# Kernel optimization log

Hardware: AMD Instinct MI355X
Metric: run time of the kernel (lower is better)

The kernel has to match this reference:

```python
import jax, jax.numpy as jnp
import numpy as np

N = 30000      # nodes
E = 480000     # edges
F = 128        # num_node_features (== C, required by LSTM-JK stacking of h_list incl. x)
C = 128        # graph_hidden_channels
K = 8          # kernel_size (num gaussians)
D = 2          # pseudo-coordinate dim
L = 4          # nlayers
H = (L * C) // 2   # PyG JK-LSTM hidden size = 256
NHID = 512
NOUT = 256
B = 1024       # number of graphs in batch
EPS = 1e-15


def setup_inputs() -> dict:
    key = jax.random.key(0)
    ks = jax.random.split(key, 24)
    s = 0.05
    inp = {}
    inp['x'] = jax.random.normal(ks[0], (N, F), jnp.float32)
    inp['edge_index'] = jax.random.randint(ks[1], (2, E), 0, N, dtype=jnp.int32)
    inp['edge_attr'] = jax.random.uniform(ks[2], (E, D), jnp.float32)
    inp['batch'] = jnp.sort(jax.random.randint(ks[3], (N,), 0, B, dtype=jnp.int32))
    # GMMConv params per layer (Cin == C for all layers since F == C)
    inp['g'] = jax.random.normal(ks[4], (L, F, K * C), jnp.float32) * s
    inp['root'] = jax.random.normal(ks[5], (L, F, C), jnp.float32) * s
    inp['bias'] = jnp.zeros((L, C), jnp.float32)
    inp['mu'] = jax.random.uniform(ks[6], (L, K, D), jnp.float32)
    inp['sigma'] = jax.random.uniform(ks[7], (L, K, D), jnp.float32) * 0.5 + 0.5
    inp['bn_gamma'] = jnp.ones((L, C), jnp.float32)
    inp['bn_beta'] = jnp.zeros((L, C), jnp.float32)
    # Bidirectional LSTM for JumpingKnowledge: dir 0 = fwd, dir 1 = bwd; gate order i,f,g,o
    inp['w_ih'] = jax.random.normal(ks[8], (2, 4 * H, C), jnp.float32) * s
    inp['w_hh'] = jax.random.normal(ks[9], (2, 4 * H, H), jnp.float32) * s
    inp['b_ih'] = jnp.zeros((2, 4 * H), jnp.float32)
    inp['b_hh'] = jnp.zeros((2, 4 * H), jnp.float32)
    inp['att_w'] = jax.random.normal(ks[10], (2 * H, 1), jnp.float32) * s
    inp['att_b'] = jnp.zeros((1,), jnp.float32)
    inp['p1_w'] = jax.random.normal(ks[11], (C, NHID), jnp.float32) * s
    inp['p1_b'] = jnp.zeros((NHID,), jnp.float32)
    inp['p2_w'] = jax.random.normal(ks[12], (NHID, NOUT), jnp.float32) * s
    inp['p2_b'] = jnp.zeros((NOUT,), jnp.float32)
    inp['ln_g'] = jnp.ones((NOUT,), jnp.float32)
    inp['ln_b'] = jnp.zeros((NOUT,), jnp.float32)
    return inp


def _lstm_dir(xs, w_ih, w_hh, b_ih, b_hh, reverse):
    # xs: [T, N, C] -> hidden states [T, N, H], aligned with input order
    def step(carry, xt):
        h, c = carry
        gates = xt @ w_ih.T + h @ w_hh.T + (b_ih + b_hh)
        i, f, g, o = jnp.split(gates, 4, axis=-1)
        c = jax.nn.sigmoid(f) * c + jax.nn.sigmoid(i) * jnp.tanh(g)
        h = jax.nn.sigmoid(o) * jnp.tanh(c)
        return (h, c), h
    h0 = jnp.zeros((xs.shape[1], w_hh.shape[1]), xs.dtype)
    _, hs = jax.lax.scan(step, (h0, h0), xs, reverse=reverse)
    return hs


def reference(x, edge_index, edge_attr, batch, g, root, bias, mu, sigma,
              bn_gamma, bn_beta, w_ih, w_hh, b_ih, b_hh, att_w, att_b,
              p1_w, p1_b, p2_w, p2_b, ln_g, ln_b):
    src, dst = edge_index[0], edge_index[1]
    deg = jnp.maximum(jax.ops.segment_sum(jnp.ones((E,), x.dtype), dst, num_segments=N), 1.0)[:, None]
    h = x
    h_list = [x]
    for i in range(L):
        # GMMConv: node-level transform then gaussian-weighted message passing (mean aggr)
        xg = (h @ g[i]).reshape(N, K, C)                     # [N, K, C]
        diff = edge_attr[:, None, :] - mu[i][None]           # [E, K, D]
        w = jnp.exp(jnp.sum(-0.5 * diff ** 2 / (EPS + sigma[i][None] ** 2), axis=-1))  # [E, K]
        msg = jnp.zeros((E, C), x.dtype)
        for k in range(K):                                   # small fixed K; avoids [E,K,C] gather
            msg = msg + w[:, k:k + 1] * xg[src, k, :]
        agg = jax.ops.segment_sum(msg, dst, num_segments=N) / deg
        h = agg + h @ root[i] + bias[i]
        # BatchNorm1d (training-mode batch statistics)
        mean = h.mean(0)
        var = h.var(0)
        h = (h - mean) / jnp.sqrt(var + 1e-5) * bn_gamma[i] + bn_beta[i]
        if i < L - 1:
            h = jax.nn.relu(h)
        # dropout is identity in eval mode
        h_list.append(h)
    # JumpingKnowledge, mode='lstm'
    xs = jnp.stack(h_list, axis=0)                           # [L+1, N, C]
    hf = _lstm_dir(xs, w_ih[0], w_hh[0], b_ih[0], b_hh[0], False)
    hb = _lstm_dir(xs, w_ih[1], w_hh[1], b_ih[1], b_hh[1], True)
    seq = jnp.concatenate([hf, hb], axis=-1)                 # [L+1, N, 2H]
    alpha = (seq @ att_w)[..., 0] + att_b[0]                 # [L+1, N]
    alpha = jax.nn.softmax(alpha, axis=0)
    node_rep = jnp.sum(alpha[..., None] * xs, axis=0)        # [N, C]
    # global_mean_pool
    cnt = jnp.maximum(jax.ops.segment_sum(jnp.ones((N,), x.dtype), batch, num_segments=B), 1.0)
    h_graph = jax.ops.segment_sum(node_rep, batch, num_segments=B) / cnt[:, None]
    z = jax.nn.relu(h_graph @ p1_w + p1_b)
    z = z @ p2_w + p2_b
    zm = z.mean(-1, keepdims=True)
    zv = z.var(-1, keepdims=True)
    return (z - zm) / jnp.sqrt(zv + 1e-5) * ln_g + ln_b
```

## Files before the change

kernel.cpp:

```cpp
#include <hip/hip_runtime.h>
#include <hip/hip_bf16.h>
#include <math.h>

#define N_    30000
#define E_    480000
#define C_    128
#define K_    8
#define L_    4
#define H_    256
#define NHID_ 512
#define NOUT_ 256
#define B_    1024
#define SCAN_B 30

typedef __attribute__((ext_vector_type(8))) short short8;
typedef __attribute__((ext_vector_type(4))) float floatx4;
typedef __hip_bfloat16 bf16;

static inline size_t align256(size_t x){ return (x + 255) & ~(size_t)255; }

__device__ __forceinline__ void gload_lds16(const void* g, void* l){
  __builtin_amdgcn_global_load_lds((const __attribute__((address_space(1))) void*)g,
                                   (__attribute__((address_space(3))) void*)l, 16, 0, 0);
}
__device__ __forceinline__ float bf2f(short s){
  union { unsigned u; float f; } x; x.u = ((unsigned)(unsigned short)s) << 16; return x.f;
}
__device__ __forceinline__ float sigm_f(float x){ return __builtin_amdgcn_rcpf(1.f + __expf(-x)); }
__device__ __forceinline__ float tanh_f(float x){ return 1.f - 2.f*__builtin_amdgcn_rcpf(1.f + __expf(2.f*x)); }

__global__ void hist_k(const int* __restrict__ dst, int* __restrict__ cnt){
  int e = blockIdx.x*256 + threadIdx.x;
  if (e < E_) atomicAdd(&cnt[dst[e]], 1);
}

__global__ void scan1_k(const int* __restrict__ cnt, int* __restrict__ rowptr, int* __restrict__ btot){
  __shared__ int sh[1024];
  int i = blockIdx.x*1024 + (int)threadIdx.x;
  int v = (i < N_) ? cnt[i] : 0;
  sh[threadIdx.x] = v;
  __syncthreads();
  for (int o = 1; o < 1024; o <<= 1){
    int t = (threadIdx.x >= (unsigned)o) ? sh[threadIdx.x - o] : 0;
    __syncthreads();
    sh[threadIdx.x] += t;
    __syncthreads();
  }
  if (i < N_) rowptr[i] = sh[threadIdx.x] - v;
  if (threadIdx.x == 1023) btot[blockIdx.x] = sh[1023];
}
__global__ void scan2_k(const int* __restrict__ btot, int* __restrict__ boff){
  if (threadIdx.x == 0){
    int s = 0;
    for (int b = 0; b < SCAN_B; b++){ boff[b] = s; s += btot[b]; }
    boff[SCAN_B] = s;
  }
}
__global__ void scan3_k(int* __restrict__ rowptr, const int* __restrict__ boff){
  int i = blockIdx.x*1024 + (int)threadIdx.x;
  if (i < N_) rowptr[i] += boff[blockIdx.x];
  if (i == N_-1) rowptr[N_] = boff[SCAN_B];
}

__global__ void degf_k(const int* __restrict__ cnt, float* __restrict__ degf){
  int n = blockIdx.x*256 + threadIdx.x;
  if (n < N_) degf[n] = fmaxf((float)cnt[n], 1.0f);
}

__global__ void scatter_k(const int* __restrict__ src, const int* __restrict__ dst,
                          const float* __restrict__ ea,
                          const int* __restrict__ rowptr, int* __restrict__ fill,
                          int* __restrict__ srcsort, float* __restrict__ easort){
  int e = blockIdx.x*256 + threadIdx.x;
  if (e >= E_) return;
  int d = dst[e];
  int pos = rowptr[d] + atomicAdd(&fill[d], 1);
  srcsort[pos] = src[e];
  ((float2*)easort)[pos] = ((const float2*)ea)[e];
}

__global__ void cast_k(const float* __restrict__ in, bf16* __restrict__ out, int n){
  int i = blockIdx.x*256 + threadIdx.x;
  if (i < n) out[i] = __float2bfloat16(in[i]);
}
__global__ void tcast_k(const float* __restrict__ in, bf16* __restrict__ out, int R, int Cc){
  const float* ip = in + (size_t)blockIdx.y*R*Cc;
  bf16* op = out + (size_t)blockIdx.y*R*Cc;
  int i = blockIdx.x*256 + threadIdx.x;
  if (i >= R*Cc) return;
  int c = i / R, r = i - c*R;
  op[i] = __float2bfloat16(ip[(size_t)r*Cc + c]);
}
__global__ void gtcast_k(const float* __restrict__ in, bf16* __restrict__ out){
  const float* ip = in + (size_t)blockIdx.y*C_*(K_*C_);
  bf16* op = out + (size_t)blockIdx.y*C_*(K_*C_);
  int i = blockIdx.x*256 + threadIdx.x;
  int co = i >> 10;
  int rem = i & 1023;
  int k = rem >> 7, c = rem & 127;
  op[i] = __float2bfloat16(ip[(size_t)c*(K_*C_) + k*C_ + co]);
}
__global__ void permcast_k(const float* __restrict__ in, bf16* __restrict__ out, int Kdim){
  const float* ip = in + (size_t)blockIdx.y*1024*Kdim;
  bf16* op = out + (size_t)blockIdx.y*1024*Kdim;
  int i = blockIdx.x*256 + threadIdx.x;
  if (i >= 1024*Kdim) return;
  int r = i / Kdim, k = i - r*Kdim;
  int gsel = r >> 8, jj = r & 255;
  int p = ((jj >> 5) << 7) + (((jj >> 4) & 1) << 6) + (gsel << 4) + (jj & 15);
  op[(size_t)p*Kdim + k] = __float2bfloat16(ip[i]);
}
__global__ void biassum_k(const float* __restrict__ bih, const float* __restrict__ bhh,
                          float* __restrict__ bs){
  int i = blockIdx.x*256 + threadIdx.x;
  if (i < 2048) bs[i] = bih[i] + bhh[i];
}

template<int OUTBF16>
__global__ __launch_bounds__(256)
void gemm_bf16_k(const bf16* __restrict__ A1, const bf16* __restrict__ B1, int K1,
                 const bf16* __restrict__ A2, const bf16* __restrict__ B2, int K2,
                 const float* __restrict__ bias1,
                 void* __restrict__ Cout, int M, int Nn, int relu)
{
  __shared__ short As[128*32];
  __shared__ short Bs[128*32];
  const int tid  = threadIdx.x;
  const int wave = tid >> 6, lane = tid & 63;
  const int m0 = blockIdx.y*128, n0 = blockIdx.x*128;
  const int wm = (wave >> 1)*64, wn = (wave & 1)*64;
  const int lrow = lane & 15, lk = lane >> 4;
  floatx4 acc[4][4] = {};

  #pragma unroll
  for (int phase = 0; phase < 2; ++phase){
    const bf16* A = phase ? A2 : A1;
    const bf16* B = phase ? B2 : B1;
    const int   K = phase ? K2 : K1;
    if (A == nullptr) continue;
    for (int k0 = 0; k0 < K; k0 += 32){
      #pragma unroll
      for (int i = 0; i < 2; ++i){
        const int c    = i*256 + wave*64 + lane;
        const int row  = c >> 2;
        const int jsrc = (c & 3) ^ ((c >> 3) & 3);
        int ar = m0 + row; if (ar >= M) ar = M - 1;
        gload_lds16(A + (size_t)ar*K + k0 + jsrc*8,         As + (size_t)c*8);
        gload_lds16(B + (size_t)(n0 + row)*K + k0 + jsrc*8, Bs + (size_t)c*8);
      }
      __syncthreads();
      short8 af[4], bfr[4];
      #pragma unroll
      for (int t = 0; t < 4; ++t){
        const int ra = wm + t*16 + lrow;
        const int rb = wn + t*16 + lrow;
        af[t]  = *(const short8*)&As[(ra*4 + (lk ^ ((ra >> 1) & 3)))*8];
        bfr[t] = *(const short8*)&Bs[(rb*4 + (lk ^ ((rb >> 1) & 3)))*8];
      }
      #pragma unroll
      for (int mt = 0; mt < 4; ++mt)
        #pragma unroll
        for (int nt = 0; nt < 4; ++nt)
          acc[mt][nt] = __builtin_amdgcn_mfma_f32_16x16x32_bf16(af[mt], bfr[nt], acc[mt][nt], 0, 0, 0);
      __syncthreads();
    }
  }

  float* outf = (float*)Cout;
  bf16*  outb = (bf16*)Cout;
  #pragma unroll
  for (int nt = 0; nt < 4; ++nt){
    const int col = n0 + wn + nt*16 + lrow;
    float bv = bias1 ? bias1[col] : 0.f;
    #pragma unroll
    for (int mt = 0; mt < 4; ++mt){
      #pragma unroll
      for (int r = 0; r < 4; ++r){
        const int row = m0 + wm + mt*16 + lk*4 + r;
        if (row >= M) continue;
        float v = acc[mt][nt][r] + bv;
        if (relu) v = fmaxf(v, 0.f);
        if (OUTBF16) outb[(size_t)row*Nn + col] = __float2bfloat16(v);
        else         outf[(size_t)row*Nn + col] = v;
      }
    }
  }
}

__global__ __launch_bounds__(256)
void gmm_gemm64_k(const bf16* __restrict__ tbuf, const bf16* __restrict__ gGTl,
                  const bf16* __restrict__ hin, const bf16* __restrict__ rootTl,
                  const float* __restrict__ bias, float* __restrict__ outp,
                  float* __restrict__ stats, int M)
{
  __shared__ short As[128*64];
  __shared__ short Bs[128*64];
  __shared__ float colstat[256];
  const int tid  = threadIdx.x;
  const int wave = tid >> 6, lane = tid & 63;
  const int m0 = blockIdx.x*128;
  const int wm = (wave >> 1)*64, wn = (wave & 1)*64;
  const int lrow = lane & 15, lk = lane >> 4;
  floatx4 acc[4][4] = {};
  colstat[tid] = 0.f;

  #pragma unroll
  for (int phase = 0; phase < 2; ++phase){
    const bf16* A  = phase ? hin    : tbuf;
    const bf16* B  = phase ? rootTl : gGTl;
    const int   ld = phase ? C_     : (K_*C_);
    const int   K  = phase ? C_     : (K_*C_);
    for (int k0 = 0; k0 < K; k0 += 64){
      #pragma unroll
      for (int i = 0; i < 4; ++i){
        const int c    = i*256 + wave*64 + lane;
        const int row  = c >> 3;
        const int jsrc = (c & 7) ^ (row & 7);
        int ar = m0 + row; if (ar >= M) ar = M - 1;
        gload_lds16(A + (size_t)ar*ld + k0 + jsrc*8,  As + (size_t)c*8);
        gload_lds16(B + (size_t)row*ld + k0 + jsrc*8, Bs + (size_t)c*8);
      }
      __syncthreads();
      #pragma unroll
      for (int kk = 0; kk < 2; ++kk){
        short8 af[4], bfr[4];
        #pragma unroll
        for (int t = 0; t < 4; ++t){
          const int ra = wm + t*16 + lrow;
          const int rb = wn + t*16 + lrow;
          af[t]  = *(const short8*)&As[(ra*8 + ((kk*4 + lk) ^ (ra & 7)))*8];
          bfr[t] = *(const short8*)&Bs[(rb*8 + ((kk*4 + lk) ^ (rb & 7)))*8];
        }
        #pragma unroll
        for (int mt = 0; mt < 4; ++mt)
          #pragma unroll
          for (int nt = 0; nt < 4; ++nt)
            acc[mt][nt] = __builtin_amdgcn_mfma_f32_16x16x32_bf16(af[mt], bfr[nt], acc[mt][nt], 0, 0, 0);
      }
      __syncthreads();
    }
  }

  #pragma unroll
  for (int nt = 0; nt < 4; ++nt){
    const int col = wn + nt*16 + lrow;
    const float bv = bias[col];
    float s = 0.f, s2 = 0.f;
    #pragma unroll
    for (int mt = 0; mt < 4; ++mt){
      #pragma unroll
      for (int r = 0; r < 4; ++r){
        const int row = m0 + wm + mt*16 + lk*4 + r;
        if (row >= M) continue;
        float v = acc[mt][nt][r] + bv;
        outp[(size_t)row*C_ + col] = v;
        s += v; s2 += v*v;
      }
    }
    s  += __shfl_down(s, 16);  s  += __shfl_down(s, 32);
    s2 += __shfl_down(s2, 16); s2 += __shfl_down(s2, 32);
    if (lane < 16){
      atomicAdd(&colstat[wn + nt*16 + lane], s);
      atomicAdd(&colstat[128 + wn + nt*16 + lane], s2);
    }
  }
  __syncthreads();
  if (tid < 128){
    atomicAdd(&stats[tid],       colstat[tid]);
    atomicAdd(&stats[128 + tid], colstat[128 + tid]);
  }
}

__global__ __launch_bounds__(256)
void lstm_step2_k(const bf16* __restrict__ A1f, const bf16* __restrict__ A1b,
                  const bf16* __restrict__ wihp, const bf16* __restrict__ whhp,
                  const bf16* __restrict__ hpf, const bf16* __restrict__ hpb,
                  const float* __restrict__ bsum,
                  bf16* __restrict__ hof, bf16* __restrict__ hob,
                  bf16* __restrict__ csf, bf16* __restrict__ csb,
                  const float* __restrict__ attw,
                  float* __restrict__ alf, float* __restrict__ alb,
                  int M)
{
  __shared__ short As[128*32];
  __shared__ short Bs[128*32];
  const int dir = blockIdx.z;
  const bf16* A1 = dir ? A1b : A1f;
  const bf16* A2 = dir ? hpb : hpf;
  const bf16* B1 = wihp + (size_t)dir*4*H_*C_;
  const bf16* B2 = whhp + (size_t)dir*4*H_*H_;
  bf16* hout = dir ? hob : hof;
  bf16* cst  = dir ? csb : csf;
  float* alpha = dir ? alb : alf;
  const float* bsd = bsum + (size_t)dir*4*H_;
  const float* awd = attw + (size_t)dir*H_;

  const int tid  = threadIdx.x;
  const int wave = tid >> 6, lane = tid & 63;
  const int m0 = blockIdx.y*128, n0 = blockIdx.x*128;
  const int wm = (wave >> 1)*64, wn = (wave & 1)*64;
  const int lrow = lane & 15, lk = lane >> 4;
  floatx4 acc[4][4] = {};

  #pragma unroll
  for (int phase = 0; phase < 2; ++phase){
    const bf16* A = phase ? A2 : A1;
    const bf16* B = phase ? B2 : B1;
    const int   K = phase ? H_ : C_;
    if (A == nullptr) continue;
    for (int k0 = 0; k0 < K; k0 += 32){
      #pragma unroll
      for (int i = 0; i < 2; ++i){
        const int c    = i*256 + wave*64 + lane;
        const int row  = c >> 2;
        const int jsrc = (c & 3) ^ ((c >> 3) & 3);
        int ar = m0 + row; if (ar >= M) ar = M - 1;
        gload_lds16(A + (size_t)ar*K + k0 + jsrc*8,         As + (size_t)c*8);
        gload_lds16(B + (size_t)(n0 + row)*K + k0 + jsrc*8, Bs + (size_t)c*8);
      }
      __syncthreads();
      short8 af[4], bfr[4];
      #pragma unroll
      for (int t = 0; t < 4; ++t){
        const int ra = wm + t*16 + lrow;
        const int rb = wn + t*16 + lrow;
        af[t]  = *(const short8*)&As[(ra*4 + (lk ^ ((ra >> 1) & 3)))*8];
        bfr[t] = *(const short8*)&Bs[(rb*4 + (lk ^ ((rb >> 1) & 3)))*8];
      }
      #pragma unroll
      for (int mt = 0; mt < 4; ++mt)
        #pragma unroll
        for (int nt = 0; nt < 4; ++nt)
          acc[mt][nt] = __builtin_amdgcn_mfma_f32_16x16x32_bf16(af[mt], bfr[nt], acc[mt][nt], 0, 0, 0);
      __syncthreads();
    }
  }

  const int j  = blockIdx.x*32 + (wave & 1)*16 + lrow;
  const float bi = bsd[0*H_ + j], bff = bsd[1*H_ + j];
  const float bg = bsd[2*H_ + j], bo  = bsd[3*H_ + j];
  const float aw = awd[j];
  #pragma unroll
  for (int mt = 0; mt < 4; ++mt){
    #pragma unroll
    for (int r = 0; r < 4; ++r){
      const int row = m0 + wm + mt*16 + lk*4 + r;
      const bool ok = row < M;
      const size_t idx = (size_t)row*H_ + j;
      float co = 0.f;
      if (A2 && ok) co = __bfloat162float(cst[idx]);
      float ig = sigm_f(acc[mt][0][r] + bi);
      float fg = sigm_f(acc[mt][1][r] + bff);
      float gt = tanh_f(acc[mt][2][r] + bg);
      float og = sigm_f(acc[mt][3][r] + bo);
      float cv = fg*co + ig*gt;
      float hv = og*tanh_f(cv);
      if (ok && hout){
        cst[idx]  = __float2bfloat16(cv);
        hout[idx] = __float2bfloat16(hv);
      }
      float att = ok ? hv*aw : 0.f;
      att += __shfl_xor(att, 1);
      att += __shfl_xor(att, 2);
      att += __shfl_xor(att, 4);
      att += __shfl_xor(att, 8);
      if (lrow == 0 && ok) atomicAdd(&alpha[row], att);
    }
  }
}

__global__ void compute_w_k(const float* __restrict__ easort, const float* __restrict__ mu,
                            const float* __restrict__ sigma, bf16* __restrict__ wsrt)
{
  int e = blockIdx.x*256 + threadIdx.x;
  if (e >= E_) return;
  float2 a = ((const float2*)easort)[e];
  short8 o;
  #pragma unroll
  for (int k = 0; k < 8; k++){
    float d0 = a.x - mu[2*k],  d1 = a.y - mu[2*k+1];
    float s0 = sigma[2*k],     s1 = sigma[2*k+1];
    float t = -0.5f*(d0*d0/(1e-15f + s0*s0) + d1*d1/(1e-15f + s1*s1));
    o[k] = __builtin_bit_cast(short, __float2bfloat16(expf(t)));
  }
  *(short8*)(wsrt + (size_t)e*8) = o;
}

__global__ __launch_bounds__(256)
void aggregate_t_k(const bf16* __restrict__ h, const bf16* __restrict__ wsrt,
                   const int* __restrict__ rowptr, const int* __restrict__ srcsort,
                   const float* __restrict__ degf, bf16* __restrict__ t)
{
  int node = blockIdx.x*4 + (threadIdx.x >> 6);
  int lane = threadIdx.x & 63;
  if (node >= N_) return;
  int p0 = rowptr[node], p1 = rowptr[node+1];
  float ax[8] = {}, ay[8] = {};
  for (int p = p0; p < p1; p++){
    int s = srcsort[p];
    short8 wv = *(const short8*)(wsrt + (size_t)p*8);
    float2 v = __bfloat1622float2(((const __hip_bfloat162*)(h + (size_t)s*C_))[lane]);
    #pragma unroll
    for (int k = 0; k < 8; k++){
      float wk = bf2f(wv[k]);
      ax[k] = fmaf(wk, v.x, ax[k]);
      ay[k] = fmaf(wk, v.y, ay[k]);
    }
  }
  float inv = 1.0f / degf[node];
  __hip_bfloat162* tp = (__hip_bfloat162*)(t + (size_t)node*(K_*C_));
  #pragma unroll
  for (int k = 0; k < 8; k++){
    __hip_bfloat162 o; o.x = __float2bfloat16(ax[k]*inv); o.y = __float2bfloat16(ay[k]*inv);
    tp[k*64 + lane] = o;
  }
}

__global__ void bn_apply_k(const float* __restrict__ hpre, const float* __restrict__ stats,
                           const float* __restrict__ gamma, const float* __restrict__ beta,
                           bf16* __restrict__ outp, int relu)
{
  int i = blockIdx.x*256 + threadIdx.x;
  if (i >= N_*C_) return;
  int c = i & 127;
  float mean = stats[c] * (1.0f/N_);
  float var  = stats[c+128] * (1.0f/N_) - mean*mean;
  float rstd = rsqrtf(var + 1e-5f);
  float v = (hpre[i] - mean)*rstd*gamma[c] + beta[c];
  if (relu) v = fmaxf(v, 0.f);
  outp[i] = __float2bfloat16(v);
}

__global__ void jk_pool_k(const float* __restrict__ x, const bf16* __restrict__ hlist,
                          const float* __restrict__ alpha, const int* __restrict__ batch,
                          float* __restrict__ hgraph, float* __restrict__ gcnt)
{
  int n = blockIdx.x, c = threadIdx.x;
  float a[5]; float mx = -1e30f;
  #pragma unroll
  for (int t = 0; t < 5; t++){ a[t] = alpha[(size_t)t*N_ + n]; mx = fmaxf(mx, a[t]); }
  float ssum = 0.f;
  #pragma unroll
  for (int t = 0; t < 5; t++){ a[t] = expf(a[t] - mx); ssum += a[t]; }
  float inv = 1.0f/ssum;
  float val = a[0]*inv*x[(size_t)n*C_ + c];
  #pragma unroll
  for (int t = 1; t < 5; t++)
    val = fmaf(a[t]*inv, __bfloat162float(hlist[((size_t)(t-1)*N_ + n)*C_ + c]), val);
  int bg = batch[n];
  atomicAdd(&hgraph[(size_t)bg*C_ + c], val);
  if (c == 0) atomicAdd(&gcnt[bg], 1.0f);
}

__global__ void pool_div_k(const float* __restrict__ hg, const float* __restrict__ gcnt,
                           bf16* __restrict__ hgb){
  int i = blockIdx.x*256 + threadIdx.x;
  if (i < B_*C_) hgb[i] = __float2bfloat16(hg[i] / fmaxf(gcnt[i >> 7], 1.0f));
}

__global__ __launch_bounds__(256)
void layernorm_k(float* __restrict__ z, const float* __restrict__ g, const float* __restrict__ b){
  int row = blockIdx.x, j = threadIdx.x;
  float v = z[(size_t)row*NOUT_ + j];
  float s = v, s2 = v*v;
  #pragma unroll
  for (int o = 32; o; o >>= 1){ s += __shfl_down(s, o); s2 += __shfl_down(s2, o); }
  __shared__ float sh[8];
  int w = j >> 6;
  if ((j & 63) == 0){ sh[w] = s; sh[4+w] = s2; }
  __syncthreads();
  float st  = sh[0] + sh[1] + sh[2] + sh[3];
  float st2 = sh[4] + sh[5] + sh[6] + sh[7];
  float mean = st * (1.0f/NOUT_);
  float var  = st2 * (1.0f/NOUT_) - mean*mean;
  float rstd = rsqrtf(var + 1e-5f);
  z[(size_t)row*NOUT_ + j] = (v - mean)*rstd*g[j] + b[j];
}

extern "C" void kernel_launch(void* const* d_in, const int* in_sizes, int n_in,
                              void* d_out, int out_size, void* d_ws, size_t ws_size,
                              hipStream_t stream)
{
  (void)in_sizes; (void)n_in; (void)out_size; (void)ws_size;
  const float* x     = (const float*)d_in[0];
  const int*   eidx  = (const int*)  d_in[1];
  const float* eattr = (const float*)d_in[2];
  const int*   batch = (const int*)  d_in[3];
  const float* g     = (const float*)d_in[4];
  const float* root  = (const float*)d_in[5];
  const float* bias  = (const float*)d_in[6];
  const float* mu    = (const float*)d_in[7];
  const float* sigma = (const float*)d_in[8];
  const float* bng   = (const float*)d_in[9];
  const float* bnb   = (const float*)d_in[10];
  const float* w_ih  = (const float*)d_in[11];
  const float* w_hh  = (const float*)d_in[12];
  const float* b_ih  = (const float*)d_in[13];
  const float* b_hh  = (const float*)d_in[14];
  const float* attw  = (const float*)d_in[15];
  const float* p1w   = (const float*)d_in[17];
  const float* p1b   = (const float*)d_in[18];
  const float* p2w   = (const float*)d_in[19];
  const float* p2b   = (const float*)d_in[20];
  const float* lng   = (const float*)d_in[21];
  const float* lnb   = (const float*)d_in[22];
  float* outp = (float*)d_out;

  const int* src = eidx;
  const int* dst = eidx + E_;

  size_t off = 0;
  char* wsb = (char*)d_ws;
  auto carve = [&](size_t bytes)->void*{ void* p = wsb + off; off = align256(off + bytes); return p; };
  bf16*  hlist  = (bf16*) carve((size_t)L_*N_*C_*2);
  void*  big    =         carve((size_t)N_*(K_*C_)*2);
  void*  uni    =         carve((size_t)6*N_*H_*2 + 256);
  bf16*  xb     = (bf16*) carve((size_t)N_*C_*2);
  float* alpha  = (float*)carve((size_t)(L_+1)*N_*4);
  float* hgraph = (float*)carve((size_t)B_*C_*4);
  bf16*  hgb    = (bf16*) carve((size_t)B_*C_*2);
  float* gcnt   = (float*)carve((size_t)B_*4);
  bf16*  z1b    = (bf16*) carve((size_t)B_*NHID_*2);
  float* bnstats= (float*)carve((size_t)L_*2*C_*4);
  float* degf   = (float*)carve((size_t)N_*4);
  int* cnt      = (int*)  carve((size_t)N_*4);
  int* rowptr   = (int*)  carve((size_t)(N_+1)*4);
  int* fill     = (int*)  carve((size_t)N_*4);
  int* srcsort  = (int*)  carve((size_t)E_*4);
  float* easort = (float*)carve((size_t)E_*2*4);
  int* btot     = (int*)  carve((size_t)(SCAN_B+1)*4);
  int* boff     = (int*)  carve((size_t)(SCAN_B+1)*4);
  bf16* gGT   = (bf16*)carve((size_t)L_*C_*(K_*C_)*2);
  bf16* rootT = (bf16*)carve((size_t)L_*C_*C_*2);
  bf16* wihp  = (bf16*)carve((size_t)2*4*H_*C_*2);
  bf16* whhp  = (bf16*)carve((size_t)2*4*H_*H_*2);
  float* bsum = (float*)carve((size_t)2*4*H_*4);
  bf16* p1T   = (bf16*)carve((size_t)NHID_*C_*2);
  bf16* p2T   = (bf16*)carve((size_t)NOUT_*NHID_*2);

  bf16*  wsrt   = (bf16*)uni;
  float* hpre   = (float*)((char*)uni + (size_t)E_*K_*2);
  bf16*  hAf    = (bf16*)uni;
  bf16*  hAb    = hAf + (size_t)N_*H_;
  bf16*  hBf    = hAb + (size_t)N_*H_;
  bf16*  hBb    = hBf + (size_t)N_*H_;
  bf16*  csf    = hBb + (size_t)N_*H_;
  bf16*  csb    = csf + (size_t)N_*H_;
  bf16*  tbuf   = (bf16*)big;

  hipMemsetAsync(cnt,     0, (size_t)N_*4, stream);
  hipMemsetAsync(fill,    0, (size_t)N_*4, stream);
  hipMemsetAsync(bnstats, 0, (size_t)L_*2*C_*4, stream);
  hipMemsetAsync(hgraph,  0, (size_t)B_*C_*4, stream);
  hipMemsetAsync(gcnt,    0, (size_t)B_*4, stream);
  hipMemsetAsync(alpha,   0, (size_t)(L_+1)*N_*4, stream);

  const dim3 blk(256);

  hist_k  <<<(E_+255)/256, 256, 0, stream>>>(dst, cnt);
  scan1_k <<<SCAN_B, 1024, 0, stream>>>(cnt, rowptr, btot);
  scan2_k <<<1, 64, 0, stream>>>(btot, boff);
  scan3_k <<<SCAN_B, 1024, 0, stream>>>(rowptr, boff);
  degf_k  <<<(N_+255)/256, 256, 0, stream>>>(cnt, degf);
  scatter_k<<<(E_+255)/256, 256, 0, stream>>>(src, dst, eattr, rowptr, fill, srcsort, easort);

  cast_k <<<(N_*C_+255)/256, blk, 0, stream>>>(x, xb, N_*C_);
  gtcast_k<<<dim3((C_*K_*C_)/256, L_), blk, 0, stream>>>(g, gGT);
  tcast_k<<<dim3((C_*C_+255)/256,   L_), blk, 0, stream>>>(root, rootT, C_,   C_);
  permcast_k<<<dim3((1024*C_+255)/256, 2), blk, 0, stream>>>(w_ih, wihp, C_);
  permcast_k<<<dim3((1024*H_+255)/256, 2), blk, 0, stream>>>(w_hh, whhp, H_);
  biassum_k<<<8, blk, 0, stream>>>(b_ih, b_hh, bsum);
  tcast_k<<<dim3((C_*NHID_+255)/256, 1), blk, 0, stream>>>(p1w, p1T, C_,    NHID_);
  tcast_k<<<dim3((NHID_*NOUT_+255)/256,1), blk, 0, stream>>>(p2w, p2T, NHID_, NOUT_);

  const int MB = (N_ + 127)/128;

  for (int l = 0; l < L_; l++){
    const bf16* hin = l ? (hlist + (size_t)(l-1)*N_*C_) : xb;
    compute_w_k<<<(E_+255)/256, blk, 0, stream>>>(easort, mu + (size_t)l*K_*2, sigma + (size_t)l*K_*2, wsrt);
    aggregate_t_k<<<N_/4, blk, 0, stream>>>(hin, wsrt, rowptr, srcsort, degf, tbuf);
    gmm_gemm64_k<<<dim3(MB), blk, 0, stream>>>(
        tbuf, gGT + (size_t)l*C_*K_*C_, hin, rootT + (size_t)l*C_*C_,
        bias + (size_t)l*C_, hpre, bnstats + l*2*C_, N_);
    bn_apply_k<<<(N_*C_+255)/256, blk, 0, stream>>>(hpre, bnstats + l*2*C_, bng + (size_t)l*C_, bnb + (size_t)l*C_,
                                                    hlist + (size_t)l*N_*C_, (l < L_-1) ? 1 : 0);
  }

  {
    const bf16 *hpf = nullptr, *hpb = nullptr;
    for (int s = 0; s < 5; s++){
      int tf = s, tb = 4 - s;
      const bf16* xtf = tf ? (hlist + (size_t)(tf-1)*N_*C_) : xb;
      const bf16* xtb = tb ? (hlist + (size_t)(tb-1)*N_*C_) : xb;
      bf16* hof = (s == 4) ? nullptr : ((s & 1) ? hBf : hAf);
      bf16* hob = (s == 4) ? nullptr : ((s & 1) ? hBb : hAb);
      lstm_step2_k<<<dim3(8, MB, 2), blk, 0, stream>>>(
          xtf, xtb, wihp, whhp, hpf, hpb, bsum, hof, hob, csf, csb,
          attw, alpha + (size_t)tf*N_, alpha + (size_t)tb*N_, N_);
      hpf = hof; hpb = hob;
    }
  }

  jk_pool_k<<<N_, 128, 0, stream>>>(x, hlist, alpha, batch, hgraph, gcnt);
  pool_div_k<<<(B_*C_+255)/256, blk, 0, stream>>>(hgraph, gcnt, hgb);

  gemm_bf16_k<1><<<dim3(NHID_/128, B_/128), blk, 0, stream>>>(
      hgb, p1T, C_, nullptr, nullptr, 0, p1b, z1b, B_, NHID_, 1);
  gemm_bf16_k<0><<<dim3(NOUT_/128, B_/128), blk, 0, stream>>>(
      z1b, p2T, NHID_, nullptr, nullptr, 0, p2b, outp, B_, NOUT_, 0);
  layernorm_k<<<B_, 256, 0, stream>>>(outp, lng, lnb);
}
```

Before: 1.213 ms.

## Halve GMM GEMM row tile, batch edge weights for all layers, fuse degf

The GMM GEMM tile shrinks from 128 to 64 rows per block, with each wave covering all 64 rows and 32 columns. That roughly doubles the grid (about 469 blocks instead of 235) and gives the 256 CUs more work to spread across, at the cost of more B-tile reloads per output. The Gaussian edge weights for all four layers are now computed in one kernel before the layer loop, saving three launches but using four times the scratch memory in the union buffer. The degf computation is folded into scan1_k, which removes one more launch.

```diff
diff --git a/kernel.cpp b/kernel.cpp
--- a/kernel.cpp
+++ b/kernel.cpp
@@ -34,10 +34,12 @@
   if (e < E_) atomicAdd(&cnt[dst[e]], 1);
 }
 
-__global__ void scan1_k(const int* __restrict__ cnt, int* __restrict__ rowptr, int* __restrict__ btot){
+__global__ void scan1_k(const int* __restrict__ cnt, int* __restrict__ rowptr,
+                        int* __restrict__ btot, float* __restrict__ degf){
   __shared__ int sh[1024];
   int i = blockIdx.x*1024 + (int)threadIdx.x;
   int v = (i < N_) ? cnt[i] : 0;
+  if (i < N_) degf[i] = fmaxf((float)v, 1.0f);
   sh[threadIdx.x] = v;
   __syncthreads();
   for (int o = 1; o < 1024; o <<= 1){
@@ -60,11 +62,6 @@
   int i = blockIdx.x*1024 + (int)threadIdx.x;
   if (i < N_) rowptr[i] += boff[blockIdx.x];
   if (i == N_-1) rowptr[N_] = boff[SCAN_B];
-}
-
-__global__ void degf_k(const int* __restrict__ cnt, float* __restrict__ degf){
-  int n = blockIdx.x*256 + threadIdx.x;
-  if (n < N_) degf[n] = fmaxf((float)cnt[n], 1.0f);
 }
 
 __global__ void scatter_k(const int* __restrict__ src, const int* __restrict__ dst,
@@ -193,15 +190,15 @@
                   const float* __restrict__ bias, float* __restrict__ outp,
                   float* __restrict__ stats, int M)
 {
-  __shared__ short As[128*64];
+  __shared__ short As[64*64];
   __shared__ short Bs[128*64];
   __shared__ float colstat[256];
   const int tid  = threadIdx.x;
   const int wave = tid >> 6, lane = tid & 63;
-  const int m0 = blockIdx.x*128;
-  const int wm = (wave >> 1)*64, wn = (wave & 1)*64;
+  const int m0 = blockIdx.x*64;
+  const int wn = wave*32;
   const int lrow = lane & 15, lk = lane >> 4;
-  floatx4 acc[4][4] = {};
+  floatx4 acc[4][2] = {};
   colstat[tid] = 0.f;
 
   #pragma unroll
@@ -212,47 +209,53 @@
     const int   K  = phase ? C_     : (K_*C_);
     for (int k0 = 0; k0 < K; k0 += 64){
       #pragma unroll
-      for (int i = 0; i < 4; ++i){
-        const int c    = i*256 + wave*64 + lane;
-        const int row  = c >> 3;
-        const int jsrc = (c & 7) ^ (row & 7);
-        int ar = m0 + row; if (ar >= M) ar = M - 1;
-        gload_lds16(A + (size_t)ar*ld + k0 + jsrc*8,  As + (size_t)c*8);
-        gload_lds16(B + (size_t)row*ld + k0 + jsrc*8, Bs + (size_t)c*8);
+      for (int i = 0; i < 6; ++i){
+        const int t = i*256 + wave*64 + lane;
+        if (t < 512){
+          const int c = t, row = c >> 3, jsrc = (c & 7) ^ (row & 7);
+          int ar = m0 + row; if (ar >= M) ar = M - 1;
+          gload_lds16(A + (size_t)ar*ld + k0 + jsrc*8, As + (size_t)c*8);
+        } else {
+          const int c = t - 512, row = c >> 3, jsrc = (c & 7) ^ (row & 7);
+          gload_lds16(B + (size_t)row*ld + k0 + jsrc*8, Bs + (size_t)c*8);
+        }
       }
       __syncthreads();
       #pragma unroll
       for (int kk = 0; kk < 2; ++kk){
-        short8 af[4], bfr[4];
+        short8 af[4], bfr[2];
         #pragma unroll
         for (int t = 0; t < 4; ++t){
-          const int ra = wm + t*16 + lrow;
-          const int rb = wn + t*16 + lrow;
-          af[t]  = *(const short8*)&As[(ra*8 + ((kk*4 + lk) ^ (ra & 7)))*8];
-          bfr[t] = *(const short8*)&Bs[(rb*8 + ((kk*4 + lk) ^ (rb & 7)))*8];
+          const int ra = t*16 + lrow;
+          af[t] = *(const short8*)&As[(ra*8 + ((kk*4 + lk) ^ (ra & 7)))*8];
+        }
+        #pragma unroll
+        for (int u = 0; u < 2; ++u){
+          const int rb = wn + u*16 + lrow;
+          bfr[u] = *(const short8*)&Bs[(rb*8 + ((kk*4 + lk) ^ (rb & 7)))*8];
         }
         #pragma unroll
         for (int mt = 0; mt < 4; ++mt)
           #pragma unroll
-          for (int nt = 0; nt < 4; ++nt)
-            acc[mt][nt] = __builtin_amdgcn_mfma_f32_16x16x32_bf16(af[mt], bfr[nt], acc[mt][nt], 0, 0, 0);
+          for (int u = 0; u < 2; ++u)
+            acc[mt][u] = __builtin_amdgcn_mfma_f32_16x16x32_bf16(af[mt], bfr[u], acc[mt][u], 0, 0, 0);
       }
       __syncthreads();
     }
   }
 
   #pragma unroll
-  for (int nt = 0; nt < 4; ++nt){
-    const int col = wn + nt*16 + lrow;
+  for (int u = 0; u < 2; ++u){
+    const int col = wn + u*16 + lrow;
     const float bv = bias[col];
     float s = 0.f, s2 = 0.f;
     #pragma unroll
     for (int mt = 0; mt < 4; ++mt){
       #pragma unroll
       for (int r = 0; r < 4; ++r){
-        const int row = m0 + wm + mt*16 + lk*4 + r;
+        const int row = m0 + mt*16 + lk*4 + r;
         if (row >= M) continue;
-        float v = acc[mt][nt][r] + bv;
+        float v = acc[mt][u][r] + bv;
         outp[(size_t)row*C_ + col] = v;
         s += v; s2 += v*v;
       }
@@ -260,8 +263,8 @@
     s  += __shfl_down(s, 16);  s  += __shfl_down(s, 32);
     s2 += __shfl_down(s2, 16); s2 += __shfl_down(s2, 32);
     if (lane < 16){
-      atomicAdd(&colstat[wn + nt*16 + lane], s);
-      atomicAdd(&colstat[128 + wn + nt*16 + lane], s2);
+      atomicAdd(&colstat[col], s);
+      atomicAdd(&colstat[128 + col], s2);
     }
   }
   __syncthreads();
@@ -369,21 +372,24 @@
   }
 }
 
-__global__ void compute_w_k(const float* __restrict__ easort, const float* __restrict__ mu,
-                            const float* __restrict__ sigma, bf16* __restrict__ wsrt)
+__global__ void compute_w4_k(const float* __restrict__ easort, const float* __restrict__ mu,
+                             const float* __restrict__ sigma, bf16* __restrict__ wsrt4)
 {
   int e = blockIdx.x*256 + threadIdx.x;
   if (e >= E_) return;
   float2 a = ((const float2*)easort)[e];
-  short8 o;
-  #pragma unroll
-  for (int k = 0; k < 8; k++){
-    float d0 = a.x - mu[2*k],  d1 = a.y - mu[2*k+1];
-    float s0 = sigma[2*k],     s1 = sigma[2*k+1];
-    float t = -0.5f*(d0*d0/(1e-15f + s0*s0) + d1*d1/(1e-15f + s1*s1));
-    o[k] = __builtin_bit_cast(short, __float2bfloat16(expf(t)));
-  }
-  *(short8*)(wsrt + (size_t)e*8) = o;
+  #pragma unroll
+  for (int l = 0; l < L_; l++){
+    short8 o;
+    #pragma unroll
+    for (int k = 0; k < 8; k++){
+      float d0 = a.x - mu[l*16 + 2*k],  d1 = a.y - mu[l*16 + 2*k+1];
+      float s0 = sigma[l*16 + 2*k],     s1 = sigma[l*16 + 2*k+1];
+      float t = -0.5f*(d0*d0/(1e-15f + s0*s0) + d1*d1/(1e-15f + s1*s1));
+      o[k] = __builtin_bit_cast(short, __float2bfloat16(expf(t)));
+    }
+    *(short8*)(wsrt4 + ((size_t)l*E_ + e)*8) = o;
+  }
 }
 
 __global__ __launch_bounds__(256)
@@ -538,8 +544,8 @@
   bf16* p1T   = (bf16*)carve((size_t)NHID_*C_*2);
   bf16* p2T   = (bf16*)carve((size_t)NOUT_*NHID_*2);
 
-  bf16*  wsrt   = (bf16*)uni;
-  float* hpre   = (float*)((char*)uni + (size_t)E_*K_*2);
+  bf16*  wsrt4  = (bf16*)uni;
+  float* hpre   = (float*)((char*)uni + (size_t)L_*E_*K_*2);
   bf16*  hAf    = (bf16*)uni;
   bf16*  hAb    = hAf + (size_t)N_*H_;
   bf16*  hBf    = hAb + (size_t)N_*H_;
@@ -558,10 +564,9 @@
   const dim3 blk(256);
 
   hist_k  <<<(E_+255)/256, 256, 0, stream>>>(dst, cnt);
-  scan1_k <<<SCAN_B, 1024, 0, stream>>>(cnt, rowptr, btot);
+  scan1_k <<<SCAN_B, 1024, 0, stream>>>(cnt, rowptr, btot, degf);
   scan2_k <<<1, 64, 0, stream>>>(btot, boff);
   scan3_k <<<SCAN_B, 1024, 0, stream>>>(rowptr, boff);
-  degf_k  <<<(N_+255)/256, 256, 0, stream>>>(cnt, degf);
   scatter_k<<<(E_+255)/256, 256, 0, stream>>>(src, dst, eattr, rowptr, fill, srcsort, easort);
 
   cast_k <<<(N_*C_+255)/256, blk, 0, stream>>>(x, xb, N_*C_);
@@ -573,13 +578,15 @@
   tcast_k<<<dim3((C_*NHID_+255)/256, 1), blk, 0, stream>>>(p1w, p1T, C_,    NHID_);
   tcast_k<<<dim3((NHID_*NOUT_+255)/256,1), blk, 0, stream>>>(p2w, p2T, NHID_, NOUT_);
 
+  compute_w4_k<<<(E_+255)/256, blk, 0, stream>>>(easort, mu, sigma, wsrt4);
+
   const int MB = (N_ + 127)/128;
+  const int MB64 = (N_ + 63)/64;
 
   for (int l = 0; l < L_; l++){
     const bf16* hin = l ? (hlist + (size_t)(l-1)*N_*C_) : xb;
-    compute_w_k<<<(E_+255)/256, blk, 0, stream>>>(easort, mu + (size_t)l*K_*2, sigma + (size_t)l*K_*2, wsrt);
-    aggregate_t_k<<<N_/4, blk, 0, stream>>>(hin, wsrt, rowptr, srcsort, degf, tbuf);
-    gmm_gemm64_k<<<dim3(MB), blk, 0, stream>>>(
+    aggregate_t_k<<<N_/4, blk, 0, stream>>>(hin, wsrt4 + (size_t)l*E_*K_, rowptr, srcsort, degf, tbuf);
+    gmm_gemm64_k<<<dim3(MB64), blk, 0, stream>>>(
         tbuf, gGT + (size_t)l*C_*K_*C_, hin, rootT + (size_t)l*C_*C_,
         bias + (size_t)l*C_, hpre, bnstats + l*2*C_, N_);
     bn_apply_k<<<(N_*C_+255)/256, blk, 0, stream>>>(hpre, bnstats + l*2*C_, bng + (size_t)l*C_, bnb + (size_t)l*C_,
```

After: 1.194 ms. No clear change (-1.6%).
